# Kernel tuning notes

Measured on AMD Instinct MI355X. Metric: run time of the kernel, lower is better.

## Reference

```python
import math
import jax, jax.numpy as jnp
import numpy as np

B, L, D, H, NL, V = 4, 1024, 1024, 16, 8, 32000
HD = D // H
EPS = 1e-5


def _sinusoidal_pe(length, dim):
    pos = jnp.arange(length, dtype=jnp.float32)[:, None]
    div = jnp.exp(jnp.arange(0, dim, 2, dtype=jnp.float32) * (-math.log(10000.0) / dim))
    pe = jnp.zeros((length, dim), dtype=jnp.float32)
    pe = pe.at[:, 0::2].set(jnp.sin(pos * div))
    pe = pe.at[:, 1::2].set(jnp.cos(pos * div))
    return pe


def _layer_norm(x, scale, bias):
    mu = jnp.mean(x, axis=-1, keepdims=True)
    var = jnp.mean(jnp.square(x - mu), axis=-1, keepdims=True)
    return (x - mu) * jax.lax.rsqrt(var + EPS) * scale + bias


def setup_inputs() -> dict:
    key = jax.random.key(0)
    ks = jax.random.split(key, 10)
    std = 0.02
    p = {
        "idx": jax.random.randint(ks[0], (B, L), 0, V),
        "emb": jax.random.normal(ks[1], (V, D), jnp.float32) * std,
        # per-layer stacked params (leading dim NL)
        "ln1_s": jnp.ones((NL, D), jnp.float32),
        "ln1_b": jnp.zeros((NL, D), jnp.float32),
        "wq": jax.random.normal(ks[2], (NL, D, D), jnp.float32) * std,
        "wk": jax.random.normal(ks[3], (NL, D, D), jnp.float32) * std,
        "wv": jax.random.normal(ks[4], (NL, D, D), jnp.float32) * std,
        "wo": jax.random.normal(ks[5], (NL, D, D), jnp.float32) * std,
        "ln2_s": jnp.ones((NL, D), jnp.float32),
        "ln2_b": jnp.zeros((NL, D), jnp.float32),
        "w1": jax.random.normal(ks[6], (NL, D, 4 * D), jnp.float32) * std,
        "b1": jnp.zeros((NL, 4 * D), jnp.float32),
        "w2": jax.random.normal(ks[7], (NL, 4 * D, D), jnp.float32) * std,
        "b2": jnp.zeros((NL, D), jnp.float32),
        "lnf_s": jnp.ones((D,), jnp.float32),
        "lnf_b": jnp.zeros((D,), jnp.float32),
        "head": jax.random.normal(ks[8], (D, V), jnp.float32) * std,
    }
    return p


def _forward(idx, emb, ln1_s, ln1_b, wq, wk, wv, wo, ln2_s, ln2_b, w1, b1, w2, b2, lnf_s, lnf_b, head):
    x = emb[idx] + _sinusoidal_pe(L, D)[None]  # [B,L,D]
    causal = jnp.tril(jnp.ones((L, L), dtype=bool))  # [L,L]
    neg_inf = jnp.float32(-jnp.inf)

    def block(x, p):
        (l1s, l1b, Wq, Wk, Wv, Wo, l2s, l2b, W1, B1, W2, B2) = p
        h = _layer_norm(x, l1s, l1b)
        q = (h @ Wq).reshape(B, L, H, HD)
        k = (h @ Wk).reshape(B, L, H, HD)
        v = (h @ Wv).reshape(B, L, H, HD)
        att = jnp.einsum("bihd,bjhd->bhij", q, k) / math.sqrt(HD)
        att = jnp.where(causal, att, neg_inf)
        att = jax.nn.softmax(att, axis=-1)
        y = jnp.einsum("bhij,bjhd->bihd", att, v).reshape(B, L, D)
        x = x + y @ Wo
        h = _layer_norm(x, l2s, l2b)
        x = x + jax.nn.gelu(h @ W1 + B1, approximate=False) @ W2 + B2
        return x, None

    params = (ln1_s, ln1_b, wq, wk, wv, wo, ln2_s, ln2_b, w1, b1, w2, b2)
    x, _ = jax.lax.scan(block, x, params)
    x = _layer_norm(x, lnf_s, lnf_b)
    return x @ head  # [B,L,V]


def reference(idx, emb, ln1_s, ln1_b, wq, wk, wv, wo, ln2_s, ln2_b, w1, b1, w2, b2, lnf_s, lnf_b, head):
    return _forward(idx, emb, ln1_s, ln1_b, wq, wk, wv, wo, ln2_s, ln2_b, w1, b1, w2, b2, lnf_s, lnf_b, head)
```

## Files before the change

### kernel.cpp

```cpp
#include <hip/hip_runtime.h>
#include <hip/hip_bf16.h>
#include <math.h>

typedef __bf16 bf16_t;
typedef __attribute__((ext_vector_type(8))) __bf16 bf16x8;
typedef __attribute__((ext_vector_type(4))) float f32x4;

#define B_  4
#define L_  1024
#define D_  1024
#define H_  16
#define HD_ 64
#define NL_ 8
#define V_  32000
#define FF_ 4096

__global__ __launch_bounds__(256) void embed_kernel(const int* __restrict__ idx,
                                                    const float* __restrict__ emb,
                                                    float* __restrict__ x) {
  int token = blockIdx.x;
  int l = token & (L_ - 1);
  int id = idx[token];
  const float* erow = emb + (size_t)id * D_;
  float* xrow = x + (size_t)token * D_;
  int d0 = threadIdx.x * 4;
#pragma unroll
  for (int j = 0; j < 4; ++j) {
    int d = d0 + j;
    int i = d >> 1;
    float freq = expf((float)(2 * i) * (-9.210340371976184f / (float)D_));
    float ang = (float)l * freq;
    float pe = (d & 1) ? cosf(ang) : sinf(ang);
    xrow[d] = erow[d] + pe;
  }
}

__global__ __launch_bounds__(256) void ln_kernel(const float* __restrict__ x,
                                                 const float* __restrict__ gamma,
                                                 const float* __restrict__ beta,
                                                 bf16_t* __restrict__ out) {
  int row = blockIdx.x;
  int t = threadIdx.x;
  float4 v = ((const float4*)(x + (size_t)row * D_))[t];
  float va[4] = {v.x, v.y, v.z, v.w};
  float s = va[0] + va[1] + va[2] + va[3];
  float ss = va[0]*va[0] + va[1]*va[1] + va[2]*va[2] + va[3]*va[3];
#pragma unroll
  for (int m = 1; m < 64; m <<= 1) {
    s  += __shfl_xor(s, m);
    ss += __shfl_xor(ss, m);
  }
  __shared__ float red[8];
  int wid = t >> 6, lane = t & 63;
  if (lane == 0) { red[wid] = s; red[4 + wid] = ss; }
  __syncthreads();
  s  = red[0] + red[1] + red[2] + red[3];
  ss = red[4] + red[5] + red[6] + red[7];
  float mu  = s * (1.0f / D_);
  float var = fmaxf(ss * (1.0f / D_) - mu * mu, 0.0f);
  float rstd = rsqrtf(var + 1e-5f);
  int d0 = t * 4;
  bf16_t* orow = out + (size_t)row * D_ + d0;
#pragma unroll
  for (int j = 0; j < 4; ++j) {
    int d = d0 + j;
    orow[j] = (bf16_t)((va[j] - mu) * rstd * gamma[d] + beta[d]);
  }
}

__global__ void transpose_k(const float* __restrict__ in, size_t base,
                            bf16_t* __restrict__ out, int K, int N, int ldin) {
  __shared__ bf16_t tile[32][33];
  int n0 = blockIdx.x * 32, k0 = blockIdx.y * 32;
#pragma unroll
  for (int r = 0; r < 4; ++r) {
    int kk = threadIdx.y + r * 8;
    tile[kk][threadIdx.x] = (bf16_t)in[base + (size_t)(k0 + kk) * ldin + n0 + threadIdx.x];
  }
  __syncthreads();
#pragma unroll
  for (int r = 0; r < 4; ++r) {
    int nn = threadIdx.y + r * 8;
    out[(size_t)(n0 + nn) * K + k0 + threadIdx.x] = tile[threadIdx.x][nn];
  }
}

__global__ void transpose_qkv(const float* __restrict__ wq,
                              const float* __restrict__ wk,
                              const float* __restrict__ wv, size_t base,
                              bf16_t* __restrict__ out) {
  const float* in = (blockIdx.z == 0) ? wq : (blockIdx.z == 1) ? wk : wv;
  __shared__ bf16_t tile[32][33];
  int n0 = blockIdx.x * 32, k0 = blockIdx.y * 32;
#pragma unroll
  for (int r = 0; r < 4; ++r) {
    int kk = threadIdx.y + r * 8;
    tile[kk][threadIdx.x] = (bf16_t)in[base + (size_t)(k0 + kk) * D_ + n0 + threadIdx.x];
  }
  __syncthreads();
  bf16_t* o = out + (size_t)blockIdx.z * D_ * D_;
#pragma unroll
  for (int r = 0; r < 4; ++r) {
    int nn = threadIdx.y + r * 8;
    o[(size_t)(n0 + nn) * D_ + k0 + threadIdx.x] = tile[threadIdx.x][nn];
  }
}

__device__ __forceinline__ void gload_lds16(const bf16_t* g, bf16_t* lds) {
  __builtin_amdgcn_global_load_lds(
      (const __attribute__((address_space(1))) void*)g,
      (__attribute__((address_space(3))) void*)(void*)lds,
      16, 0, 0);
}

__device__ __forceinline__ void remap_block(int& bn, int& bm) {
  const int gx = gridDim.x, gy = gridDim.y;
  int lin = blockIdx.y * gx + blockIdx.x;
  int nwg = gx * gy;
  int q8 = nwg >> 3, r8 = nwg & 7;
  int xcd = lin & 7, pos = lin >> 3;
  int wg = (xcd < r8 ? xcd * (q8 + 1) : r8 * (q8 + 1) + (xcd - r8) * q8) + pos;
  if ((gy & 7) == 0) {
    int per = gx << 3;
    int grp = wg / per, win = wg % per;
    bm = (grp << 3) + (win & 7);
    bn = win >> 3;
  } else { bn = wg % gx; bm = wg / gx; }
}

template <int EPI>
__global__ __launch_bounds__(256) void gemm_bt_kernel(
    const bf16_t* __restrict__ A, const bf16_t* __restrict__ Bt,
    bf16_t* __restrict__ outb, float* __restrict__ outf,
    const float* __restrict__ bias, int M, int Nst, int K, int col0) {
  int bn, bm; remap_block(bn, bm);
  const int tid = threadIdx.x, wid = tid >> 6, lane = tid & 63;
  const int wm = wid >> 1, wn = wid & 1;
  const int l15 = lane & 15, l4 = lane >> 4;

  __shared__ __align__(16) bf16_t As[128 * 32];
  __shared__ __align__(16) bf16_t Bs[128 * 32];

  f32x4 acc[4][4] = {};

  const bf16_t* Ablk = A  + (size_t)(bm * 128) * K;
  const bf16_t* Bblk = Bt + (size_t)(bn * 128) * K;
  const int srow = lane >> 2;
  const int skof = (lane & 3) * 8;

  for (int k0 = 0; k0 < K; k0 += 32) {
#pragma unroll
    for (int c = 0; c < 2; ++c) {
      int chunk = wid * 2 + c;
      int row = chunk * 16 + srow;
      gload_lds16(Ablk + (size_t)row * K + k0 + skof, As + chunk * 512);
      gload_lds16(Bblk + (size_t)row * K + k0 + skof, Bs + chunk * 512);
    }
    __syncthreads();

    bf16x8 af[4], bfv[4];
#pragma unroll
    for (int i = 0; i < 4; ++i)
      af[i] = *(const bf16x8*)(As + (wm * 64 + i * 16 + l15) * 32 + l4 * 8);
#pragma unroll
    for (int j = 0; j < 4; ++j)
      bfv[j] = *(const bf16x8*)(Bs + (wn * 64 + j * 16 + l15) * 32 + l4 * 8);
#pragma unroll
    for (int i = 0; i < 4; ++i)
#pragma unroll
      for (int j = 0; j < 4; ++j)
        acc[i][j] = __builtin_amdgcn_mfma_f32_16x16x32_bf16(af[i], bfv[j], acc[i][j], 0, 0, 0);
    __syncthreads();
  }

  const int row_base = bm * 128 + wm * 64;
  const int col_base = col0 + bn * 128 + wn * 64 + l15;
#pragma unroll
  for (int i = 0; i < 4; ++i) {
#pragma unroll
    for (int j = 0; j < 4; ++j) {
      int col = col_base + j * 16;
#pragma unroll
      for (int r = 0; r < 4; ++r) {
        int row = row_base + i * 16 + l4 * 4 + r;
        float val = acc[i][j][r];
        if (EPI == 1) {
          outf[(size_t)row * Nst + col] += val;
        } else {
          outf[(size_t)row * Nst + col] += val + bias[col];
        }
      }
    }
  }
}

template <int EPI>
__global__ __launch_bounds__(512, 2) void gemm256_kernel(
    const bf16_t* __restrict__ A, const bf16_t* __restrict__ Bt,
    bf16_t* __restrict__ outb, float* __restrict__ outf,
    const float* __restrict__ bias, int M, int Nst, int K, int col0) {
  int bn, bm; remap_block(bn, bm);
  const int tid = threadIdx.x, wid = tid >> 6, lane = tid & 63;
  const int wm = wid >> 2, wn = wid & 3;
  const int l15 = lane & 15, l4 = lane >> 4;

  __shared__ __align__(16) bf16_t smem[65536];

  f32x4 acc[8][4] = {};

  const bf16_t* Ab = A  + (size_t)(bm * 256) * K;
  const bf16_t* Bb = Bt + (size_t)(bn * 256) * K;
  const int NT = K >> 6;

  const int srow = tid >> 3;
  const int sxs  = (tid & 7) ^ (srow & 7);
  const int xrd  = l15 & 7;

  auto stage = [&](int t, int pbuf) {
    const size_t kq = (size_t)t * 64 + sxs * 8;
    const bf16_t* ga = Ab + (size_t)srow * K + kq;
    const bf16_t* gb = Bb + (size_t)srow * K + kq;
    bf16_t* la = smem + pbuf * 32768 + wid * 512;
    bf16_t* lb = la + 16384;
#pragma unroll
    for (int c = 0; c < 4; ++c)
      gload_lds16(gb + (size_t)(c * 64) * K, lb + c * 4096);
    gload_lds16(ga,                       la);
    gload_lds16(ga + (size_t)128 * K,     la + 2 * 4096);
    gload_lds16(ga + (size_t)64 * K,      la + 1 * 4096);
    gload_lds16(ga + (size_t)192 * K,     la + 3 * 4096);
  };

  stage(0, 0);
  asm volatile("s_waitcnt vmcnt(2)" ::: "memory");
  __builtin_amdgcn_s_barrier();

  for (int t = 0; t < NT; ++t) {
    const int pb = t & 1;
    const bf16_t* sA = smem + pb * 32768;
    const bf16_t* sB = sA + 16384;
    const bool pre = (t + 1 < NT);
    if (pre) stage(t + 1, pb ^ 1);

    bf16x8 bfr[4][2];
#pragma unroll
    for (int n = 0; n < 4; ++n)
#pragma unroll
      for (int ks = 0; ks < 2; ++ks)
        bfr[n][ks] = *(const bf16x8*)(sB + (wn * 64 + n * 16 + l15) * 64
                                         + ((ks * 4 + l4) ^ xrd) * 8);

#pragma unroll
    for (int mh = 0; mh < 4; ++mh) {
      if (mh == 2) {
        if (pre) { asm volatile("s_waitcnt vmcnt(8)" ::: "memory"); }
        else     { asm volatile("s_waitcnt vmcnt(0)" ::: "memory"); }
        __builtin_amdgcn_s_barrier();
      }
      bf16x8 af[2][2];
#pragma unroll
      for (int m = 0; m < 2; ++m)
#pragma unroll
        for (int ks = 0; ks < 2; ++ks)
          af[m][ks] = *(const bf16x8*)(sA + (wm * 128 + (mh * 2 + m) * 16 + l15) * 64
                                          + ((ks * 4 + l4) ^ xrd) * 8);
      __builtin_amdgcn_s_setprio(1);
#pragma unroll
      for (int m = 0; m < 2; ++m)
#pragma unroll
        for (int n = 0; n < 4; ++n)
#pragma unroll
          for (int ks = 0; ks < 2; ++ks)
            acc[mh * 2 + m][n] = __builtin_amdgcn_mfma_f32_16x16x32_bf16(
                af[m][ks], bfr[n][ks], acc[mh * 2 + m][n], 0, 0, 0);
      __builtin_amdgcn_s_setprio(0);
    }

    if (pre) { asm volatile("s_waitcnt vmcnt(2)" ::: "memory"); }
    __builtin_amdgcn_s_barrier();
  }

  const int row_base = bm * 256 + wm * 128;
#pragma unroll
  for (int m = 0; m < 8; ++m) {
#pragma unroll
    for (int n = 0; n < 4; ++n) {
      int colg = bn * 256 + wn * 64 + n * 16 + l15;
#pragma unroll
      for (int r = 0; r < 4; ++r) {
        int row = row_base + m * 16 + l4 * 4 + r;
        float val = acc[m][n][r];
        if (EPI == 4) {
          outf[(size_t)row * Nst + col0 + colg] = val;
        } else if (EPI == 2) {
          int col = col0 + colg;
          float v2 = val + bias[col];
          v2 = 0.5f * v2 * (1.0f + erff(v2 * 0.7071067811865475f));
          outb[(size_t)row * Nst + col] = (bf16_t)v2;
        } else {
          int buf = colg >> 10;
          int lc  = colg & 1023;
          (outb + (size_t)buf * 4194304)[(size_t)row * 1024 + lc] = (bf16_t)val;
        }
      }
    }
  }
}

__global__ __launch_bounds__(256) void attn_kernel(
    const bf16_t* __restrict__ q, const bf16_t* __restrict__ k,
    const bf16_t* __restrict__ v, bf16_t* __restrict__ y) {
  int bid = blockIdx.x;
  int qt = bid & 15;
  int h  = (bid >> 4) & (H_ - 1);
  int b  = bid >> 8;
  int tid = threadIdx.x, wid = tid >> 6, lane = tid & 63;
  int l15 = lane & 15, l4 = lane >> 4;

  __shared__ __align__(16) bf16_t Ks[64 * 72];
  __shared__ __align__(16) bf16_t Vs[64 * 72];
  __shared__ __align__(16) bf16_t Ps[4][16 * 72];

  const int qrow0 = qt * 64 + wid * 16;
  const size_t bh = ((size_t)b * L_ * H_ + h) * HD_;

  bf16x8 qf[2];
#pragma unroll
  for (int c = 0; c < 2; ++c)
    qf[c] = *(const bf16x8*)(q + bh + (size_t)(qrow0 + l15) * (H_ * HD_) + c * 32 + l4 * 8);

  float m_r[4] = {-INFINITY, -INFINITY, -INFINITY, -INFINITY};
  float l_r[4] = {0.f, 0.f, 0.f, 0.f};
  f32x4 oacc[4] = {};

  for (int kt = 0; kt <= qt; ++kt) {
    __syncthreads();
    int kbase = kt * 64;
#pragma unroll
    for (int s = 0; s < 2; ++s) {
      int seg = s * 256 + tid;
      int j = seg >> 3;
      int dof = (seg & 7) * 8;
      const size_t src = bh + (size_t)(kbase + j) * (H_ * HD_) + dof;
      *(bf16x8*)(Ks + j * 72 + dof) = *(const bf16x8*)(k + src);
      bf16x8 vv = *(const bf16x8*)(v + src);
      int colb = (j + dof) & 63;
#pragma unroll
      for (int jj = 0; jj < 8; ++jj) Vs[(dof + jj) * 72 + colb] = vv[jj];
    }
    __syncthreads();

    f32x4 sacc[4] = {};
#pragma unroll
    for (int c = 0; c < 2; ++c) {
#pragma unroll
      for (int t = 0; t < 4; ++t) {
        bf16x8 kf = *(const bf16x8*)(Ks + (t * 16 + l15) * 72 + c * 32 + l4 * 8);
        sacc[t] = __builtin_amdgcn_mfma_f32_16x16x32_bf16(qf[c], kf, sacc[t], 0, 0, 0);
      }
    }

    float tmax[4] = {-INFINITY, -INFINITY, -INFINITY, -INFINITY};
#pragma unroll
    for (int t = 0; t < 4; ++t) {
#pragma unroll
      for (int r = 0; r < 4; ++r) {
        float sv = sacc[t][r] * 0.125f;
        int kj = kbase + t * 16 + l15;
        int qi = qrow0 + l4 * 4 + r;
        if (kj > qi) sv = -INFINITY;
        sacc[t][r] = sv;
        tmax[r] = fmaxf(tmax[r], sv);
      }
    }
#pragma unroll
    for (int r = 0; r < 4; ++r) {
#pragma unroll
      for (int md = 1; md < 16; md <<= 1)
        tmax[r] = fmaxf(tmax[r], __shfl_xor(tmax[r], md));
    }
    float alpha[4], tsum[4];
#pragma unroll
    for (int r = 0; r < 4; ++r) {
      float mn = fmaxf(m_r[r], tmax[r]);
      alpha[r] = expf(m_r[r] - mn);
      m_r[r] = mn;
      tsum[r] = 0.f;
    }
#pragma unroll
    for (int t = 0; t < 4; ++t) {
#pragma unroll
      for (int r = 0; r < 4; ++r) {
        float p = expf(sacc[t][r] - m_r[r]);
        tsum[r] += p;
        Ps[wid][(l4 * 4 + r) * 72 + t * 16 + l15] = (bf16_t)p;
      }
    }
#pragma unroll
    for (int r = 0; r < 4; ++r) {
#pragma unroll
      for (int md = 1; md < 16; md <<= 1)
        tsum[r] += __shfl_xor(tsum[r], md);
      l_r[r] = l_r[r] * alpha[r] + tsum[r];
    }
#pragma unroll
    for (int t = 0; t < 4; ++t)
#pragma unroll
      for (int r = 0; r < 4; ++r)
        oacc[t][r] *= alpha[r];

#pragma unroll
    for (int c = 0; c < 2; ++c) {
      bf16x8 pf = *(const bf16x8*)(&Ps[wid][l15 * 72 + c * 32 + l4 * 8]);
#pragma unroll
      for (int t = 0; t < 4; ++t) {
        int d = t * 16 + l15;
        int jb = c * 32 + l4 * 8;
        bf16x8 vf = *(const bf16x8*)(Vs + d * 72 + ((jb + (d & 56)) & 63));
        oacc[t] = __builtin_amdgcn_mfma_f32_16x16x32_bf16(pf, vf, oacc[t], 0, 0, 0);
      }
    }
  }

#pragma unroll
  for (int t = 0; t < 4; ++t) {
#pragma unroll
    for (int r = 0; r < 4; ++r) {
      int row = qrow0 + l4 * 4 + r;
      int d = t * 16 + l15;
      y[bh + (size_t)row * (H_ * HD_) + d] = (bf16_t)(oacc[t][r] / l_r[r]);
    }
  }
}

extern "C" void kernel_launch(void* const* d_in, const int* in_sizes, int n_in,
                              void* d_out, int out_size, void* d_ws, size_t ws_size,
                              hipStream_t stream) {
  (void)in_sizes; (void)n_in; (void)out_size;
  const int*   idx   = (const int*)d_in[0];
  const float* emb   = (const float*)d_in[1];
  const float* ln1_s = (const float*)d_in[2];
  const float* ln1_b = (const float*)d_in[3];
  const float* wq    = (const float*)d_in[4];
  const float* wk    = (const float*)d_in[5];
  const float* wv    = (const float*)d_in[6];
  const float* wo    = (const float*)d_in[7];
  const float* ln2_s = (const float*)d_in[8];
  const float* ln2_b = (const float*)d_in[9];
  const float* w1    = (const float*)d_in[10];
  const float* b1    = (const float*)d_in[11];
  const float* w2    = (const float*)d_in[12];
  const float* b2    = (const float*)d_in[13];
  const float* lnf_s = (const float*)d_in[14];
  const float* lnf_b = (const float*)d_in[15];
  const float* headw = (const float*)d_in[16];
  float* out = (float*)d_out;

  char* ws = (char*)d_ws;
  const size_t XO  = 0;
  const size_t HBO = XO  + 16777216;
  const size_t QBO = HBO + 8388608;
  const size_t KBO = QBO + 8388608;
  const size_t VBO = KBO + 8388608;
  const size_t YBO = VBO + 8388608;
  const size_t GBO = QBO;
  const size_t WTO = YBO + 8388608;

  float*  X  = (float*)(ws + XO);
  bf16_t* Hb = (bf16_t*)(ws + HBO);
  bf16_t* Qb = (bf16_t*)(ws + QBO);
  bf16_t* Kb = (bf16_t*)(ws + KBO);
  bf16_t* Vb = (bf16_t*)(ws + VBO);
  bf16_t* Yb = (bf16_t*)(ws + YBO);
  bf16_t* Gb = (bf16_t*)(ws + GBO);
  bf16_t* WT = (bf16_t*)(ws + WTO);

  const int M = B_ * L_;
  const dim3 tb(32, 8);

  embed_kernel<<<M, 256, 0, stream>>>(idx, emb, X);

  for (int l = 0; l < NL_; ++l) {
    const size_t wof = (size_t)l * D_ * D_;
    ln_kernel<<<M, 256, 0, stream>>>(X, ln1_s + (size_t)l * D_, ln1_b + (size_t)l * D_, Hb);

    transpose_qkv<<<dim3(D_/32, D_/32, 3), tb, 0, stream>>>(wq, wk, wv, wof, WT);
    gemm256_kernel<5><<<dim3(3*D_/256, M/256), 512, 0, stream>>>(Hb, WT, Qb, nullptr, nullptr, M, D_, D_, 0);

    attn_kernel<<<B_ * H_ * (L_/64), 256, 0, stream>>>(Qb, Kb, Vb, Yb);

    transpose_k<<<dim3(D_/32, D_/32), tb, 0, stream>>>(wo, wof, WT, D_, D_, D_);
    gemm_bt_kernel<1><<<dim3(D_/128, M/128), 256, 0, stream>>>(Yb, WT, nullptr, X, nullptr, M, D_, D_, 0);

    ln_kernel<<<M, 256, 0, stream>>>(X, ln2_s + (size_t)l * D_, ln2_b + (size_t)l * D_, Hb);

    transpose_k<<<dim3(FF_/32, D_/32), tb, 0, stream>>>(w1, (size_t)l * D_ * FF_, WT, D_, FF_, FF_);
    gemm256_kernel<2><<<dim3(FF_/256, M/256), 512, 0, stream>>>(Hb, WT, Gb, nullptr, b1 + (size_t)l * FF_, M, FF_, D_, 0);

    transpose_k<<<dim3(D_/32, FF_/32), tb, 0, stream>>>(w2, (size_t)l * FF_ * D_, WT, FF_, D_, D_);
    gemm_bt_kernel<3><<<dim3(D_/128, M/128), 256, 0, stream>>>(Gb, WT, nullptr, X, b2 + (size_t)l * D_, M, D_, FF_, 0);
  }

  ln_kernel<<<M, 256, 0, stream>>>(X, lnf_s, lnf_b, Hb);

  size_t avail = (ws_size > WTO) ? (ws_size - WTO) : 0;
  long long maxcols = (long long)(avail / ((size_t)D_ * 2));
  int chunk = (int)((maxcols / 256) * 256);
  if (chunk > V_) chunk = V_;
  if (chunk < 256) chunk = 256;
  for (int n0 = 0; n0 < V_; n0 += chunk) {
    int nc = (V_ - n0 < chunk) ? (V_ - n0) : chunk;
    transpose_k<<<dim3(nc/32, D_/32), tb, 0, stream>>>(headw, (size_t)n0, WT, D_, nc, V_);
    gemm256_kernel<4><<<dim3(nc/256, M/256), 512, 0, stream>>>(Hb, WT, nullptr, out, nullptr, M, V_, D_, n0);
  }
}
```

Baseline: 3.018 ms.

## Halve gemm256 K-tile to 32 with smaller LDS double buffer

The 256x256 GEMM kernel now stages K-tiles of 32 instead of 64. This halves shared memory from 128KB to 64KB, changes the XOR swizzle to a 4-slot pattern, and removes the mid-tile split wait/barrier. The aim is to lower LDS footprint, possibly improving occupancy, and to simplify the pipeline. In exchange it doubles the number of iterations and barriers, and each tile waits for all loads to finish (vmcnt(0)), which reduces overlap of loads with compute.

```diff
diff --git a/kernel.cpp b/kernel.cpp
--- a/kernel.cpp
+++ b/kernel.cpp
@@ -204,79 +204,57 @@
   const int wm = wid >> 2, wn = wid & 3;
   const int l15 = lane & 15, l4 = lane >> 4;
 
-  __shared__ __align__(16) bf16_t smem[65536];
+  __shared__ __align__(16) bf16_t smem[32768];
 
   f32x4 acc[8][4] = {};
 
   const bf16_t* Ab = A  + (size_t)(bm * 256) * K;
   const bf16_t* Bb = Bt + (size_t)(bn * 256) * K;
-  const int NT = K >> 6;
-
-  const int srow = tid >> 3;
-  const int sxs  = (tid & 7) ^ (srow & 7);
-  const int xrd  = l15 & 7;
+  const int NT = K >> 5;
+
+  const int srow16 = lane >> 2;
+  const int sslot  = lane & 3;
+  const int xrd    = l15 & 3;
 
   auto stage = [&](int t, int pbuf) {
-    const size_t kq = (size_t)t * 64 + sxs * 8;
-    const bf16_t* ga = Ab + (size_t)srow * K + kq;
-    const bf16_t* gb = Bb + (size_t)srow * K + kq;
-    bf16_t* la = smem + pbuf * 32768 + wid * 512;
-    bf16_t* lb = la + 16384;
-#pragma unroll
-    for (int c = 0; c < 4; ++c)
-      gload_lds16(gb + (size_t)(c * 64) * K, lb + c * 4096);
-    gload_lds16(ga,                       la);
-    gload_lds16(ga + (size_t)128 * K,     la + 2 * 4096);
-    gload_lds16(ga + (size_t)64 * K,      la + 1 * 4096);
-    gload_lds16(ga + (size_t)192 * K,     la + 3 * 4096);
+    bf16_t* base = smem + pbuf * 16384;
+#pragma unroll
+    for (int c = 0; c < 2; ++c) {
+      int row = c * 128 + wid * 16 + srow16;
+      int gs  = sslot ^ (row & 3);
+      const size_t go = (size_t)row * K + t * 32 + gs * 8;
+      gload_lds16(Bb + go, base + 8192 + c * 4096 + wid * 512);
+      gload_lds16(Ab + go, base +        c * 4096 + wid * 512);
+    }
   };
 
   stage(0, 0);
-  asm volatile("s_waitcnt vmcnt(2)" ::: "memory");
+  asm volatile("s_waitcnt vmcnt(0)" ::: "memory");
   __builtin_amdgcn_s_barrier();
 
   for (int t = 0; t < NT; ++t) {
     const int pb = t & 1;
-    const bf16_t* sA = smem + pb * 32768;
-    const bf16_t* sB = sA + 16384;
+    const bf16_t* sA = smem + pb * 16384;
+    const bf16_t* sB = sA + 8192;
     const bool pre = (t + 1 < NT);
     if (pre) stage(t + 1, pb ^ 1);
 
-    bf16x8 bfr[4][2];
+    bf16x8 bfr[4];
 #pragma unroll
     for (int n = 0; n < 4; ++n)
-#pragma unroll
-      for (int ks = 0; ks < 2; ++ks)
-        bfr[n][ks] = *(const bf16x8*)(sB + (wn * 64 + n * 16 + l15) * 64
-                                         + ((ks * 4 + l4) ^ xrd) * 8);
-
-#pragma unroll
-    for (int mh = 0; mh < 4; ++mh) {
-      if (mh == 2) {
-        if (pre) { asm volatile("s_waitcnt vmcnt(8)" ::: "memory"); }
-        else     { asm volatile("s_waitcnt vmcnt(0)" ::: "memory"); }
-        __builtin_amdgcn_s_barrier();
-      }
-      bf16x8 af[2][2];
-#pragma unroll
-      for (int m = 0; m < 2; ++m)
-#pragma unroll
-        for (int ks = 0; ks < 2; ++ks)
-          af[m][ks] = *(const bf16x8*)(sA + (wm * 128 + (mh * 2 + m) * 16 + l15) * 64
-                                          + ((ks * 4 + l4) ^ xrd) * 8);
-      __builtin_amdgcn_s_setprio(1);
-#pragma unroll
-      for (int m = 0; m < 2; ++m)
-#pragma unroll
-        for (int n = 0; n < 4; ++n)
-#pragma unroll
-          for (int ks = 0; ks < 2; ++ks)
-            acc[mh * 2 + m][n] = __builtin_amdgcn_mfma_f32_16x16x32_bf16(
-                af[m][ks], bfr[n][ks], acc[mh * 2 + m][n], 0, 0, 0);
-      __builtin_amdgcn_s_setprio(0);
-    }
-
-    if (pre) { asm volatile("s_waitcnt vmcnt(2)" ::: "memory"); }
+      bfr[n] = *(const bf16x8*)(sB + (wn * 64 + n * 16 + l15) * 32 + ((l4 ^ xrd) & 3) * 8);
+
+    __builtin_amdgcn_s_setprio(1);
+#pragma unroll
+    for (int m = 0; m < 8; ++m) {
+      bf16x8 af = *(const bf16x8*)(sA + (wm * 128 + m * 16 + l15) * 32 + ((l4 ^ xrd) & 3) * 8);
+#pragma unroll
+      for (int n = 0; n < 4; ++n)
+        acc[m][n] = __builtin_amdgcn_mfma_f32_16x16x32_bf16(af, bfr[n], acc[m][n], 0, 0, 0);
+    }
+    __builtin_amdgcn_s_setprio(0);
+
+    if (pre) { asm volatile("s_waitcnt vmcnt(0)" ::: "memory"); }
     __builtin_amdgcn_s_barrier();
   }
 
```

New measurement: 3.124 ms. 3.5% more time.
